# Optimization experiments

Measured on AMD Instinct MI355X. Metric: run time of the kernel, lower is better.

Reference implementation:

```python
import jax, jax.numpy as jnp
import numpy as np

SHIFTS = (1, 2, 4, 8)
NL = 8  # num_layer: 8 fixed contrast kernels


def _base_kernels():
    d1 = np.array([[[-1, 0, 0], [0, 1, 0], [0, 0, 0]],
                   [[0, -1, 0], [0, 1, 0], [0, 0, 0]],
                   [[0, 0, -1], [0, 1, 0], [0, 0, 0]],
                   [[0, 0, 0], [0, 1, -1], [0, 0, 0]]], dtype=np.float32).reshape(4, 1, 3, 3)
    d2 = d1[:, :, ::-1, ::-1].copy()
    k = np.concatenate([d1, d2], axis=0)      # [8,1,3,3] fixed contrast kernels
    k0 = k.mean(0, keepdims=True)             # [1,1,3,3] mean kernel (kernel0)
    return jnp.asarray(k), jnp.asarray(k0)


def _depthwise(x, w, dilation):
    # x: [B,C,H,W], w: [C,1,3,3]; torch conv2d(padding='same', groups=C, dilation=d)
    return jax.lax.conv_general_dilated(
        x, w, window_strides=(1, 1), padding='SAME',
        rhs_dilation=(dilation, dilation),
        dimension_numbers=('NCHW', 'OIHW', 'NCHW'),
        feature_group_count=x.shape[1])


def _l2norm(x, eps=1e-12):
    # F.normalize(dim=-1): x / max(||x||_2, eps)
    n = jnp.sqrt(jnp.sum(x * x, axis=-1, keepdims=True))
    return x / jnp.maximum(n, eps)


def setup_inputs() -> dict:
    key = jax.random.key(0)
    ks = jax.random.split(key, 8)
    B, C, H, W = 8, 64, 96, 96
    nh = len(SHIFTS)
    hid = C // nh
    return {
        'cen': jax.random.normal(ks[0], (B, C, H, W), jnp.float32),
        'sum_weights': jax.random.normal(ks[1], (nh, C, 1, 1, 1, 2), jnp.float32),
        'q_w': jax.random.normal(ks[2], (nh, hid, C), jnp.float32) / np.sqrt(C),
        'k_w': jax.random.normal(ks[3], (nh, NL * hid, NL * C), jnp.float32) / np.sqrt(NL * C),
        'v_w': jax.random.normal(ks[4], (nh, NL * hid, NL * C), jnp.float32) / np.sqrt(NL * C),
        'out_w': jax.random.normal(ks[5], (C, C), jnp.float32) / np.sqrt(C),
        'bn_gamma': jnp.ones((C,), jnp.float32),
        'bn_beta': jnp.zeros((C,), jnp.float32),
    }


def reference(cen, sum_weights, q_w, k_w, v_w, out_w, bn_gamma, bn_beta):
    b, c, h, w = cen.shape
    nh = len(SHIFTS)
    K, K0 = _base_kernels()  # [8,1,3,3], [1,1,3,3]

    keys, qrys, vals = [], [], []
    for i, s in enumerate(SHIFTS):
        sw = jax.nn.softmax(sum_weights[i], axis=-1)  # [C,1,1,1,2]
        # mixed kernels: kernel_j*sw0 + kernel0*sw1 per channel -> [8,C,1,3,3]
        mixed = K[:, None] * sw[None, ..., 0] + K0[:, None] * sw[None, ..., 1]
        # 8 depthwise dilated convs, vmapped over the 8 kernels -> [8,B,C,H,W]
        surr = jax.vmap(lambda kw: _depthwise(cen, kw, s))(mixed)
        # torch.cat along channels in kernel-major order (j, c)
        surr = jnp.transpose(surr, (1, 0, 2, 3, 4)).reshape(b, NL * c, h, w)
        keys.append(jnp.einsum('oc,bchw->bohw', k_w[i], surr))
        vals.append(jnp.einsum('oc,bchw->bohw', v_w[i], surr))
        qrys.append(jnp.einsum('oc,bchw->bohw', q_w[i], cen))

    # torch: stack(dim=2).view(b, nh, -1, h*w)  (raw row-major reinterpret)
    keys = jnp.stack(keys, axis=2).reshape(b, nh, -1, h * w)
    qrys = jnp.stack(qrys, axis=2).reshape(b, nh, -1, h * w)
    vals = jnp.stack(vals, axis=2).reshape(b, nh, -1, h * w)

    k_n = _l2norm(keys)  # L2 norm over spatial axis
    q_n = _l2norm(qrys)
    # scores: [b, heads, hid, 8*hid]
    scores = jnp.einsum('bhqs,bhks->bhqk', q_n, k_n) / jnp.sqrt(jnp.float32(h * w))
    # InstanceNorm2d(num_heads), affine=False, eps=1e-5: per (b, head) over (q, k)
    mu = scores.mean(axis=(-2, -1), keepdims=True)
    var = scores.var(axis=(-2, -1), keepdims=True)
    attn = jax.nn.softmax((scores - mu) * jax.lax.rsqrt(var + 1e-5), axis=-1)
    out = jnp.einsum('bhqk,bhks->bhqs', attn, vals).reshape(b, c, h, w)

    # out_conv: 1x1 conv (no bias) + BatchNorm2d (train-mode batch stats) + ReLU
    y = jnp.einsum('oc,bchw->bohw', out_w, out)
    m = y.mean(axis=(0, 2, 3), keepdims=True)
    v2 = y.var(axis=(0, 2, 3), keepdims=True)
    y = (y - m) * jax.lax.rsqrt(v2 + 1e-5)
    y = y * bn_gamma[None, :, None, None] + bn_beta[None, :, None, None]
    return jax.nn.relu(y)
```

## Files before the change

### kernel.cpp

```cpp
#include <hip/hip_runtime.h>
#include <hip/hip_bf16.h>


#define WS_CEN    0UL
#define WS_SPART  12845056UL
#define WS_W      25690112UL
#define WS_Q      28049408UL
#define WS_KV     46923776UL
#define WS_KKP    197918720UL
#define WS_QQP    198213632UL
#define WS_ATTN   198250496UL
#define WS_OUT    198512640UL
#define WS_BN     217387008UL

typedef __attribute__((ext_vector_type(8))) short short8;
typedef __attribute__((ext_vector_type(4))) float f32x4;

__device__ __forceinline__ float bflo(unsigned int u){ return __uint_as_float(u<<16); }
__device__ __forceinline__ float bfhi(unsigned int u){ return __uint_as_float(u & 0xffff0000u); }
__device__ __forceinline__ unsigned short f2bf(float f){
  unsigned int u = __float_as_uint(f);
  return (unsigned short)((u + 0x7fffu + ((u>>16)&1u)) >> 16);
}
__device__ __forceinline__ unsigned short fbits(float f){
  __hip_bfloat16 h = __float2bfloat16(f);
  return __builtin_bit_cast(unsigned short, h);
}

__global__ __launch_bounds__(256) void pad_kernel(const float* __restrict__ cen, unsigned short* __restrict__ cenbf){
  int idx = blockIdx.x*256 + threadIdx.x;
  int px = idx % 112; int t = idx / 112; int py = t % 112; int bc = t / 112;
  int y = py - 8, x = px - 8;
  float v = 0.f;
  if (y >= 0 && y < 96 && x >= 0 && x < 96) v = cen[(size_t)bc*9216 + y*96 + x];
  cenbf[idx] = fbits(v);
}

__global__ __launch_bounds__(256) void prep_kernel(const float* __restrict__ sumw,
    const float* __restrict__ kw, const float* __restrict__ vw, unsigned short* __restrict__ Wb){
  int idx = blockIdx.x*256 + threadIdx.x;
  int o = idx & 255; int r = idx >> 8; int c = r & 63; r >>= 6; int t = r % 9; int i = r / 9;
  float l0 = sumw[(i*64 + c)*2 + 0], l1 = sumw[(i*64 + c)*2 + 1];
  float m = fmaxf(l0, l1);
  float e0 = expf(l0 - m), e1 = expf(l1 - m);
  float inv = 1.f/(e0 + e1);
  float sw0 = e0*inv, sw1 = e1*inv;
  const float* wsrc = (o < 128) ? (kw + ((size_t)i*128 + o)*512 + c)
                                : (vw + ((size_t)i*128 + (o-128))*512 + c);
  float A = 0.f;
  #pragma unroll
  for (int j = 0; j < 8; ++j) A += wsrc[j*64];
  float val;
  if (t == 4) {
    val = A;
  } else {
    const int tmap[9] = {0,1,2,7,0,3,6,5,4};
    int j = tmap[t];
    val = -(wsrc[j*64]*sw0 + A*sw1*0.125f);
  }
  int k = t*64 + c;
  Wb[(((size_t)i*18 + (k>>5))*256 + o)*32 + (k&31)] = f2bf(val);
}

__global__ __launch_bounds__(256) void qproj_kernel(const float* __restrict__ cen,
    const float* __restrict__ qw, unsigned short* __restrict__ qbf){
  __shared__ float WT[64][64];
  int tid = threadIdx.x;
  int st = blockIdx.x, b = blockIdx.y;
  #pragma unroll
  for (int e = 0; e < 16; ++e) {
    int f = e*256 + tid; int c = f >> 6, row = f & 63;
    int i = row & 3, o = row >> 2;
    WT[c][row] = qw[(size_t)i*1024 + o*64 + c];
  }
  __syncthreads();
  int s = st*256 + tid;
  float acc[64];
  #pragma unroll
  for (int r = 0; r < 64; ++r) acc[r] = 0.f;
  const float* cb = cen + (size_t)b*64*9216 + s;
  for (int c = 0; c < 64; ++c) {
    float xv = cb[(size_t)c*9216];
    #pragma unroll
    for (int r4 = 0; r4 < 16; ++r4) {
      float4 w = *(const float4*)&WT[c][r4*4];
      acc[r4*4+0] = fmaf(w.x, xv, acc[r4*4+0]);
      acc[r4*4+1] = fmaf(w.y, xv, acc[r4*4+1]);
      acc[r4*4+2] = fmaf(w.z, xv, acc[r4*4+2]);
      acc[r4*4+3] = fmaf(w.w, xv, acc[r4*4+3]);
    }
  }
  unsigned short* qb = qbf + (size_t)b*64*9216 + s;
  #pragma unroll
  for (int r = 0; r < 64; ++r) qb[(size_t)r*9216] = fbits(acc[r]);
}

__global__ __launch_bounds__(512, 2) void conv_kv_mfma(const unsigned short* __restrict__ cenbf,
    const unsigned short* __restrict__ Wb, unsigned short* __restrict__ KV){
  __shared__ char Xs[2][256*72];
  const int tid = threadIdx.x;
  const int st = blockIdx.x, ib = blockIdx.z;
  const int i = ib >> 3, b = ib & 7;
  const int dil = 1 << i;
  const int s0 = st*256;
  const int wave = tid >> 6, lane = tid & 63;
  const int wm = wave >> 2, wn = wave & 3;
  const int l15 = lane & 15, l4 = lane >> 4;
  const int s_idx = tid & 255;
  const int khalf = tid >> 8;
  const int s = s0 + s_idx;
  const int y = s / 96, x = s - y*96;
  const unsigned short* cb = cenbf + (size_t)b*802816 + (size_t)(y+8)*112 + (x+8);

  f32x4 acc[8][4];
  #pragma unroll
  for (int mf = 0; mf < 8; ++mf)
    #pragma unroll
    for (int nf = 0; nf < 4; ++nf)
      acc[mf][nf] = (f32x4){0.f, 0.f, 0.f, 0.f};

  const unsigned short* Wi = Wb + (size_t)i*18*8192;
  const unsigned short* apb = Wi + (size_t)(wm*128 + l15)*32 + l4*8;

  unsigned short vs[16];
  auto gather = [&](int kn){
    int t = kn >> 1;
    int cbase = (kn & 1)*32 + khalf*16;
    int dy = (t/3 - 1)*dil, dx = (t - (t/3)*3 - 1)*dil;
    const unsigned short* p = cb + (size_t)cbase*12544 + (dy*112 + dx);
    #pragma unroll
    for (int j = 0; j < 16; ++j) vs[j] = p[(size_t)j*12544];
  };

  gather(0);
  int buf = 0;
  for (int kc = 0; kc < 18; ++kc) {
    short8 a[8];
    const unsigned short* ap = apb + (size_t)kc*8192;
    #pragma unroll
    for (int mf = 0; mf < 8; ++mf) a[mf] = *(const short8*)(ap + mf*512);
    asm volatile("" ::: "memory");
    char* wp = Xs[buf] + s_idx*72 + khalf*32;
    #pragma unroll
    for (int w = 0; w < 4; ++w) {
      unsigned int p0 = (unsigned int)vs[4*w+0] | ((unsigned int)vs[4*w+1] << 16);
      unsigned int p1 = (unsigned int)vs[4*w+2] | ((unsigned int)vs[4*w+3] << 16);
      *(uint2*)(wp + w*8) = make_uint2(p0, p1);
    }
    if (kc < 17) gather(kc + 1);
    asm volatile("s_waitcnt lgkmcnt(0)" ::: "memory");
    __builtin_amdgcn_s_barrier();
    asm volatile("" ::: "memory");
    short8 bfr[4];
    #pragma unroll
    for (int nf = 0; nf < 4; ++nf) {
      const char* rp = Xs[buf] + (wn*64 + nf*16 + l15)*72 + l4*16;
      uint2 lo = *(const uint2*)rp;
      uint2 hi = *(const uint2*)(rp + 8);
      uint4 tb = make_uint4(lo.x, lo.y, hi.x, hi.y);
      bfr[nf] = *(short8*)&tb;
    }
    #pragma unroll
    for (int mf = 0; mf < 8; ++mf)
      #pragma unroll
      for (int nf = 0; nf < 4; ++nf)
        acc[mf][nf] = __builtin_amdgcn_mfma_f32_16x16x32_bf16(a[mf], bfr[nf], acc[mf][nf], 0, 0, 0);
    buf ^= 1;
  }

  #pragma unroll
  for (int mf = 0; mf < 8; ++mf) {
    #pragma unroll
    for (int nf = 0; nf < 4; ++nf) {
      int scol = s0 + wn*64 + nf*16 + l15;
      int obase = wm*128 + mf*16 + l4*4;
      #pragma unroll
      for (int r = 0; r < 4; ++r)
        KV[((size_t)ib*256 + obase + r)*9216 + scol] = fbits(acc[mf][nf][r]);
    }
  }
}

__global__ __launch_bounds__(256) void scores_mfma(const unsigned short* __restrict__ KV,
    const unsigned short* __restrict__ qbf, float* __restrict__ spart,
    float* __restrict__ kkpart, float* __restrict__ qqpart){
  __shared__ float red[4][2192];
  const int tid = threadIdx.x;
  const int chunk = blockIdx.x, hh = blockIdx.y, b = blockIdx.z;
  const int wave = tid >> 6, lane = tid & 63;
  const int l15 = lane & 15, l4 = lane >> 4;
  const int sbase = chunk*512 + wave*128;

  const unsigned short* qp = qbf + ((size_t)(b*64 + hh*16 + l15))*9216 + sbase + l4*8;
  const unsigned short* kp = KV + ((size_t)(((l15&3)*8 + b)*256 + hh*32 + (l15>>2)))*9216 + sbase + l4*8;

  f32x4 sacc[8], kkacc[8], qqacc;
  #pragma unroll
  for (int nf = 0; nf < 8; ++nf) { sacc[nf] = (f32x4){0,0,0,0}; kkacc[nf] = (f32x4){0,0,0,0}; }
  qqacc = (f32x4){0,0,0,0};

  #pragma unroll
  for (int sl = 0; sl < 4; ++sl) {
    short8 qf = *(const short8*)(qp + sl*32);
    short8 kf[8];
    #pragma unroll
    for (int nf = 0; nf < 8; ++nf) kf[nf] = *(const short8*)(kp + (size_t)nf*36864 + sl*32);
    qqacc = __builtin_amdgcn_mfma_f32_16x16x32_bf16(qf, qf, qqacc, 0, 0, 0);
    #pragma unroll
    for (int nf = 0; nf < 8; ++nf) {
      sacc[nf]  = __builtin_amdgcn_mfma_f32_16x16x32_bf16(qf, kf[nf], sacc[nf], 0, 0, 0);
      kkacc[nf] = __builtin_amdgcn_mfma_f32_16x16x32_bf16(kf[nf], kf[nf], kkacc[nf], 0, 0, 0);
    }
  }
  float* rw = red[wave];
  #pragma unroll
  for (int nf = 0; nf < 8; ++nf)
    #pragma unroll
    for (int r = 0; r < 4; ++r)
      rw[(l4*4 + r)*128 + nf*16 + l15] = sacc[nf][r];
  if ((l15 >> 2) == l4) {
    int r = l15 & 3;
    #pragma unroll
    for (int nf = 0; nf < 8; ++nf) rw[2048 + nf*16 + l15] = kkacc[nf][r];
    rw[2176 + l15] = qqacc[r];
  }
  __syncthreads();
  int pb = (b*4 + hh)*18 + chunk;
  for (int t = tid; t < 2192; t += 256) {
    float v = red[0][t] + red[1][t] + red[2][t] + red[3][t];
    if (t < 2048)       spart[(size_t)pb*2048 + t] = v;
    else if (t < 2176)  kkpart[(size_t)pb*128 + (t - 2048)] = v;
    else                qqpart[(size_t)pb*16 + (t - 2176)] = v;
  }
}

__global__ __launch_bounds__(256) void softmax_kernel(const float* __restrict__ spart,
    const float* __restrict__ kkpart, const float* __restrict__ qqpart, float* __restrict__ attnT){
  const int pb = blockIdx.x, tid = threadIdx.x;
  const int qr = tid >> 4, g = tid & 15;
  __shared__ float kkl[128];
  __shared__ float qql[16];
  __shared__ float red[8];
  __shared__ float stats[2];
  float sv[8] = {0,0,0,0,0,0,0,0};
  for (int ch = 0; ch < 18; ++ch) {
    const float* p = spart + ((size_t)(pb*18 + ch))*2048 + qr*128 + g*8;
    #pragma unroll
    for (int e = 0; e < 8; ++e) sv[e] += p[e];
  }
  if (tid < 128) { float ssum = 0.f; for (int ch = 0; ch < 18; ++ch) ssum += kkpart[(size_t)(pb*18+ch)*128 + tid]; kkl[tid] = ssum; }
  if (tid < 16)  { float ssum = 0.f; for (int ch = 0; ch < 18; ++ch) ssum += qqpart[(size_t)(pb*18+ch)*16 + tid]; qql[tid] = ssum; }
  __syncthreads();
  float qn = fmaxf(sqrtf(qql[qr]), 1e-12f);
  float lsum = 0.f, lsq = 0.f;
  #pragma unroll
  for (int e = 0; e < 8; ++e) {
    float kn = fmaxf(sqrtf(kkl[g*8+e]), 1e-12f);
    float v = sv[e] / (qn * kn * 96.0f);
    sv[e] = v; lsum += v; lsq += v*v;
  }
  #pragma unroll
  for (int m = 1; m <= 32; m <<= 1) { lsum += __shfl_xor(lsum, m); lsq += __shfl_xor(lsq, m); }
  if ((tid & 63) == 0) { red[tid >> 6] = lsum; red[4 + (tid >> 6)] = lsq; }
  __syncthreads();
  if (tid == 0) {
    float ts = red[0]+red[1]+red[2]+red[3];
    float tq = red[4]+red[5]+red[6]+red[7];
    float mean = ts / 2048.0f;
    float var = tq / 2048.0f - mean*mean;
    stats[0] = mean; stats[1] = rsqrtf(var + 1e-5f);
  }
  __syncthreads();
  float mean = stats[0], inv = stats[1];
  float mx = -1e30f;
  #pragma unroll
  for (int e = 0; e < 8; ++e) { sv[e] = (sv[e] - mean) * inv; mx = fmaxf(mx, sv[e]); }
  #pragma unroll
  for (int m = 1; m <= 8; m <<= 1) mx = fmaxf(mx, __shfl_xor(mx, m));
  float es = 0.f;
  #pragma unroll
  for (int e = 0; e < 8; ++e) { sv[e] = expf(sv[e] - mx); es += sv[e]; }
  #pragma unroll
  for (int m = 1; m <= 8; m <<= 1) es += __shfl_xor(es, m);
  float rinv = 1.0f / es;
  #pragma unroll
  for (int e = 0; e < 8; ++e) attnT[(size_t)pb*2048 + (g*8+e)*16 + qr] = sv[e] * rinv;
}

__global__ __launch_bounds__(256) void pv_kernel(const unsigned short* __restrict__ KV,
    const float* __restrict__ attnT, float* __restrict__ outbuf){
  __shared__ float at[128][16];
  int tid = threadIdx.x;
  int st = blockIdx.x, hh = blockIdx.y, b = blockIdx.z;
  const float* ap = attnT + ((size_t)(b*4 + hh))*2048;
  #pragma unroll
  for (int e = 0; e < 8; ++e) ((float*)at)[e*256 + tid] = ap[e*256 + tid];
  __syncthreads();
  int sbase = st*1024 + tid*4;
  float acc[16][4];
  #pragma unroll
  for (int q = 0; q < 16; ++q)
    #pragma unroll
    for (int p = 0; p < 4; ++p) acc[q][p] = 0.f;
  #pragma unroll 2
  for (int kr = 0; kr < 128; ++kr) {
    int ii = kr & 3, oo = 128 + hh*32 + (kr >> 2);
    const unsigned short* vp = KV + ((size_t)((ii*8 + b)*256 + oo))*9216 + sbase;
    uint2 u = *(const uint2*)vp;
    float v0 = bflo(u.x), v1 = bfhi(u.x), v2 = bflo(u.y), v3 = bfhi(u.y);
    #pragma unroll
    for (int q4 = 0; q4 < 4; ++q4) {
      float4 a = *(const float4*)&at[kr][q4*4];
      float av[4] = {a.x, a.y, a.z, a.w};
      #pragma unroll
      for (int j = 0; j < 4; ++j) {
        acc[q4*4+j][0] = fmaf(av[j], v0, acc[q4*4+j][0]);
        acc[q4*4+j][1] = fmaf(av[j], v1, acc[q4*4+j][1]);
        acc[q4*4+j][2] = fmaf(av[j], v2, acc[q4*4+j][2]);
        acc[q4*4+j][3] = fmaf(av[j], v3, acc[q4*4+j][3]);
      }
    }
  }
  float* ob = outbuf + ((size_t)(b*64 + hh*16))*9216 + sbase;
  #pragma unroll
  for (int q = 0; q < 16; ++q) {
    float4 w = make_float4(acc[q][0], acc[q][1], acc[q][2], acc[q][3]);
    *(float4*)(ob + (size_t)q*9216) = w;
  }
}

__global__ __launch_bounds__(256) void outconv_kernel(const float* __restrict__ outbuf,
    const float* __restrict__ ow, float* __restrict__ dout){
  __shared__ float WT[64][64];
  int tid = threadIdx.x; int st = blockIdx.x; int b = blockIdx.y;
  #pragma unroll
  for (int e = 0; e < 16; ++e) {
    int f = e*256 + tid; int c = f >> 6, o = f & 63;
    WT[c][o] = ow[o*64 + c];
  }
  __syncthreads();
  int s = st*256 + tid;
  float acc[64];
  #pragma unroll
  for (int o = 0; o < 64; ++o) acc[o] = 0.f;
  for (int c = 0; c < 64; ++c) {
    float xv = outbuf[((size_t)(b*64 + c))*9216 + s];
    #pragma unroll
    for (int o4 = 0; o4 < 16; ++o4) {
      float4 w = *(const float4*)&WT[c][o4*4];
      acc[o4*4+0] = fmaf(w.x, xv, acc[o4*4+0]);
      acc[o4*4+1] = fmaf(w.y, xv, acc[o4*4+1]);
      acc[o4*4+2] = fmaf(w.z, xv, acc[o4*4+2]);
      acc[o4*4+3] = fmaf(w.w, xv, acc[o4*4+3]);
    }
  }
  #pragma unroll
  for (int o = 0; o < 64; ++o) dout[((size_t)(b*64 + o))*9216 + s] = acc[o];
}

__global__ __launch_bounds__(256) void bnstats_kernel(const float* __restrict__ yb, float* __restrict__ bnpart){
  int o = blockIdx.x, qt = blockIdx.y, tid = threadIdx.x;
  float s = 0.f, sq = 0.f;
  for (int k = tid; k < 18432; k += 256) {
    int f = qt*18432 + k;
    int b = f / 9216, sp = f - b*9216;
    float v = yb[((size_t)(b*64 + o))*9216 + sp];
    s += v; sq += v*v;
  }
  #pragma unroll
  for (int m = 1; m <= 32; m <<= 1) { s += __shfl_xor(s, m); sq += __shfl_xor(sq, m); }
  __shared__ float r0[4], r1[4];
  if ((tid & 63) == 0) { r0[tid >> 6] = s; r1[tid >> 6] = sq; }
  __syncthreads();
  if (tid == 0) {
    bnpart[qt*128 + o]      = r0[0]+r0[1]+r0[2]+r0[3];
    bnpart[qt*128 + 64 + o] = r1[0]+r1[1]+r1[2]+r1[3];
  }
}

__global__ __launch_bounds__(256) void bnapply_kernel(float* __restrict__ yb,
    const float* __restrict__ bnpart, const float* __restrict__ gamma, const float* __restrict__ beta){
  int gid = blockIdx.x*256 + threadIdx.x;
  int o = (gid / 2304) & 63;
  float ts = 0.f, tq = 0.f;
  #pragma unroll
  for (int qt = 0; qt < 4; ++qt) { ts += bnpart[qt*128 + o]; tq += bnpart[qt*128 + 64 + o]; }
  float mean = ts * (1.f/73728.f);
  float var = tq * (1.f/73728.f) - mean*mean;
  float inv = rsqrtf(var + 1e-5f);
  float g = gamma[o], be = beta[o];
  float4 v = ((const float4*)yb)[gid];
  v.x = fmaxf((v.x - mean)*inv*g + be, 0.f);
  v.y = fmaxf((v.y - mean)*inv*g + be, 0.f);
  v.z = fmaxf((v.z - mean)*inv*g + be, 0.f);
  v.w = fmaxf((v.w - mean)*inv*g + be, 0.f);
  ((float4*)yb)[gid] = v;
}

extern "C" void kernel_launch(void* const* d_in, const int* in_sizes, int n_in,
                              void* d_out, int out_size, void* d_ws, size_t ws_size,
                              hipStream_t stream) {
  const float* cen   = (const float*)d_in[0];
  const float* sumw  = (const float*)d_in[1];
  const float* qw    = (const float*)d_in[2];
  const float* kw    = (const float*)d_in[3];
  const float* vw    = (const float*)d_in[4];
  const float* ow    = (const float*)d_in[5];
  const float* gamma = (const float*)d_in[6];
  const float* beta  = (const float*)d_in[7];

  char* ws = (char*)d_ws;
  unsigned short* cenbf  = (unsigned short*)(ws + WS_CEN);
  float*          spart  = (float*)(ws + WS_SPART);
  unsigned short* Wb     = (unsigned short*)(ws + WS_W);
  unsigned short* qbf    = (unsigned short*)(ws + WS_Q);
  unsigned short* KV     = (unsigned short*)(ws + WS_KV);
  float*          kkp    = (float*)(ws + WS_KKP);
  float*          qqp    = (float*)(ws + WS_QQP);
  float*          attnT  = (float*)(ws + WS_ATTN);
  float*          outbuf = (float*)(ws + WS_OUT);
  float*          bnp    = (float*)(ws + WS_BN);

  pad_kernel    <<<25088, 256, 0, stream>>>(cen, cenbf);
  prep_kernel   <<<2304, 256, 0, stream>>>(sumw, kw, vw, Wb);
  qproj_kernel  <<<dim3(36, 8), 256, 0, stream>>>(cen, qw, qbf);
  conv_kv_mfma  <<<dim3(36, 1, 32), 512, 0, stream>>>(cenbf, Wb, KV);
  scores_mfma   <<<dim3(18, 4, 8), 256, 0, stream>>>(KV, qbf, spart, kkp, qqp);
  softmax_kernel<<<32, 256, 0, stream>>>(spart, kkp, qqp, attnT);
  pv_kernel     <<<dim3(9, 4, 8), 256, 0, stream>>>(KV, attnT, outbuf);
  outconv_kernel<<<dim3(36, 8), 256, 0, stream>>>(outbuf, ow, (float*)d_out);
  bnstats_kernel<<<dim3(64, 4), 256, 0, stream>>>((const float*)d_out, bnp);
  bnapply_kernel<<<4608, 256, 0, stream>>>((float*)d_out, bnp, gamma, beta);
}
```

Before: 441.9 us.

## Fold out_conv weights into attention, fuse PV+outconv+BN stats via MFMA GEMM

Result: faster. 427.7 us (-3.2%).

```diff
diff --git a/kernel.cpp b/kernel.cpp
--- a/kernel.cpp
+++ b/kernel.cpp
@@ -10,8 +10,9 @@
 #define WS_KKP    197918720UL
 #define WS_QQP    198213632UL
 #define WS_ATTN   198250496UL
-#define WS_OUT    198512640UL
-#define WS_BN     217387008UL
+#define WS_AB     198512640UL
+#define WS_BNP    217387008UL
+#define WS_BNF    217681920UL
 
 typedef __attribute__((ext_vector_type(8))) short short8;
 typedef __attribute__((ext_vector_type(4))) float f32x4;
@@ -95,32 +96,32 @@
   for (int r = 0; r < 64; ++r) qb[(size_t)r*9216] = fbits(acc[r]);
 }
 
-__global__ __launch_bounds__(512, 2) void conv_kv_mfma(const unsigned short* __restrict__ cenbf,
+__global__ __launch_bounds__(256, 3) void conv_kv_mfma(const unsigned short* __restrict__ cenbf,
     const unsigned short* __restrict__ Wb, unsigned short* __restrict__ KV){
-  __shared__ char Xs[2][256*72];
+  __shared__ char Xs[2][128*72];
   const int tid = threadIdx.x;
-  const int st = blockIdx.x, ib = blockIdx.z;
+  const int st = blockIdx.x, oc = blockIdx.y, ib = blockIdx.z;
   const int i = ib >> 3, b = ib & 7;
   const int dil = 1 << i;
-  const int s0 = st*256;
+  const int s0 = st*128;
   const int wave = tid >> 6, lane = tid & 63;
-  const int wm = wave >> 2, wn = wave & 3;
+  const int wm = wave >> 1, wn = wave & 1;
   const int l15 = lane & 15, l4 = lane >> 4;
-  const int s_idx = tid & 255;
-  const int khalf = tid >> 8;
+  const int s_idx = tid & 127;
+  const int khalf = tid >> 7;
   const int s = s0 + s_idx;
   const int y = s / 96, x = s - y*96;
   const unsigned short* cb = cenbf + (size_t)b*802816 + (size_t)(y+8)*112 + (x+8);
 
-  f32x4 acc[8][4];
-  #pragma unroll
-  for (int mf = 0; mf < 8; ++mf)
+  f32x4 acc[4][4];
+  #pragma unroll
+  for (int mf = 0; mf < 4; ++mf)
     #pragma unroll
     for (int nf = 0; nf < 4; ++nf)
       acc[mf][nf] = (f32x4){0.f, 0.f, 0.f, 0.f};
 
   const unsigned short* Wi = Wb + (size_t)i*18*8192;
-  const unsigned short* apb = Wi + (size_t)(wm*128 + l15)*32 + l4*8;
+  const unsigned short* apb = Wi + (size_t)(oc*128 + wm*64 + l15)*32 + l4*8;
 
   unsigned short vs[16];
   auto gather = [&](int kn){
@@ -135,10 +136,10 @@
   gather(0);
   int buf = 0;
   for (int kc = 0; kc < 18; ++kc) {
-    short8 a[8];
+    short8 a[4];
     const unsigned short* ap = apb + (size_t)kc*8192;
     #pragma unroll
-    for (int mf = 0; mf < 8; ++mf) a[mf] = *(const short8*)(ap + mf*512);
+    for (int mf = 0; mf < 4; ++mf) a[mf] = *(const short8*)(ap + mf*512);
     asm volatile("" ::: "memory");
     char* wp = Xs[buf] + s_idx*72 + khalf*32;
     #pragma unroll
@@ -161,7 +162,7 @@
       bfr[nf] = *(short8*)&tb;
     }
     #pragma unroll
-    for (int mf = 0; mf < 8; ++mf)
+    for (int mf = 0; mf < 4; ++mf)
       #pragma unroll
       for (int nf = 0; nf < 4; ++nf)
         acc[mf][nf] = __builtin_amdgcn_mfma_f32_16x16x32_bf16(a[mf], bfr[nf], acc[mf][nf], 0, 0, 0);
@@ -169,11 +170,11 @@
   }
 
   #pragma unroll
-  for (int mf = 0; mf < 8; ++mf) {
+  for (int mf = 0; mf < 4; ++mf) {
     #pragma unroll
     for (int nf = 0; nf < 4; ++nf) {
       int scol = s0 + wn*64 + nf*16 + l15;
-      int obase = wm*128 + mf*16 + l4*4;
+      int obase = oc*128 + wm*64 + mf*16 + l4*4;
       #pragma unroll
       for (int r = 0; r < 4; ++r)
         KV[((size_t)ib*256 + obase + r)*9216 + scol] = fbits(acc[mf][nf][r]);
@@ -287,106 +288,124 @@
   for (int e = 0; e < 8; ++e) attnT[(size_t)pb*2048 + (g*8+e)*16 + qr] = sv[e] * rinv;
 }
 
-__global__ __launch_bounds__(256) void pv_kernel(const unsigned short* __restrict__ KV,
-    const float* __restrict__ attnT, float* __restrict__ outbuf){
-  __shared__ float at[128][16];
-  int tid = threadIdx.x;
-  int st = blockIdx.x, hh = blockIdx.y, b = blockIdx.z;
-  const float* ap = attnT + ((size_t)(b*4 + hh))*2048;
-  #pragma unroll
-  for (int e = 0; e < 8; ++e) ((float*)at)[e*256 + tid] = ap[e*256 + tid];
-  __syncthreads();
-  int sbase = st*1024 + tid*4;
-  float acc[16][4];
-  #pragma unroll
-  for (int q = 0; q < 16; ++q)
-    #pragma unroll
-    for (int p = 0; p < 4; ++p) acc[q][p] = 0.f;
-  #pragma unroll 2
-  for (int kr = 0; kr < 128; ++kr) {
-    int ii = kr & 3, oo = 128 + hh*32 + (kr >> 2);
-    const unsigned short* vp = KV + ((size_t)((ii*8 + b)*256 + oo))*9216 + sbase;
-    uint2 u = *(const uint2*)vp;
-    float v0 = bflo(u.x), v1 = bfhi(u.x), v2 = bflo(u.y), v3 = bfhi(u.y);
-    #pragma unroll
-    for (int q4 = 0; q4 < 4; ++q4) {
-      float4 a = *(const float4*)&at[kr][q4*4];
-      float av[4] = {a.x, a.y, a.z, a.w};
+__global__ __launch_bounds__(256) void attnfold_kernel(const float* __restrict__ attnT,
+    const float* __restrict__ ow, unsigned short* __restrict__ Ab){
+  int idx = blockIdx.x*256 + threadIdx.x;
+  int kr = idx & 127, hh = (idx >> 7) & 3, o2 = (idx >> 9) & 63, b = idx >> 15;
+  const float* ap = attnT + ((size_t)(b*4 + hh))*2048 + kr*16;
+  const float* wp = ow + o2*64 + hh*16;
+  float acc = 0.f;
+  #pragma unroll
+  for (int qr = 0; qr < 16; ++qr) acc += wp[qr] * ap[qr];
+  int rc = (kr & 3)*4 + hh, ch = kr >> 2;
+  Ab[(((size_t)b*16 + rc)*64 + o2)*32 + ch] = fbits(acc);
+}
+
+__global__ __launch_bounds__(256, 3) void ygemm_kernel(const unsigned short* __restrict__ KV,
+    const unsigned short* __restrict__ Ab, float* __restrict__ dout, float* __restrict__ bnpart){
+  __shared__ char Xs[2][128*72];
+  __shared__ float bns[4][32], bnq[4][32];
+  const int tid = threadIdx.x;
+  const int st = blockIdx.x, b = blockIdx.y;
+  const int wave = tid >> 6, lane = tid & 63;
+  const int wm = wave >> 1, wn = wave & 1;
+  const int l15 = lane & 15, l4 = lane >> 4;
+  const int s_idx = tid & 127, khalf = tid >> 7;
+  const int s0 = st*128;
+
+  f32x4 acc[2][4];
+  #pragma unroll
+  for (int mf = 0; mf < 2; ++mf)
+    #pragma unroll
+    for (int nf = 0; nf < 4; ++nf)
+      acc[mf][nf] = (f32x4){0.f, 0.f, 0.f, 0.f};
+
+  const unsigned short* Abb = Ab + ((size_t)b*16*64)*32 + (size_t)(wm*32 + l15)*32 + l4*8;
+
+  unsigned short vs[16];
+  auto vgather = [&](int kn){
+    int vr = (((kn >> 2)*8 + b)*256 + 128 + (kn & 3)*32) + khalf*16;
+    const unsigned short* p = KV + (size_t)vr*9216 + s0 + s_idx;
+    #pragma unroll
+    for (int j = 0; j < 16; ++j) vs[j] = p[(size_t)j*9216];
+  };
+
+  vgather(0);
+  int buf = 0;
+  for (int kc = 0; kc < 16; ++kc) {
+    short8 a[2];
+    #pragma unroll
+    for (int mf = 0; mf < 2; ++mf) a[mf] = *(const short8*)(Abb + (size_t)kc*2048 + mf*512);
+    asm volatile("" ::: "memory");
+    char* wp = Xs[buf] + s_idx*72 + khalf*32;
+    #pragma unroll
+    for (int w = 0; w < 4; ++w) {
+      unsigned int p0 = (unsigned int)vs[4*w+0] | ((unsigned int)vs[4*w+1] << 16);
+      unsigned int p1 = (unsigned int)vs[4*w+2] | ((unsigned int)vs[4*w+3] << 16);
+      *(uint2*)(wp + w*8) = make_uint2(p0, p1);
+    }
+    if (kc < 15) vgather(kc + 1);
+    asm volatile("s_waitcnt lgkmcnt(0)" ::: "memory");
+    __builtin_amdgcn_s_barrier();
+    asm volatile("" ::: "memory");
+    short8 bfr[4];
+    #pragma unroll
+    for (int nf = 0; nf < 4; ++nf) {
+      const char* rp = Xs[buf] + (wn*64 + nf*16 + l15)*72 + l4*16;
+      uint2 lo = *(const uint2*)rp;
+      uint2 hi = *(const uint2*)(rp + 8);
+      uint4 tb = make_uint4(lo.x, lo.y, hi.x, hi.y);
+      bfr[nf] = *(short8*)&tb;
+    }
+    #pragma unroll
+    for (int mf = 0; mf < 2; ++mf)
       #pragma unroll
-      for (int j = 0; j < 4; ++j) {
-        acc[q4*4+j][0] = fmaf(av[j], v0, acc[q4*4+j][0]);
-        acc[q4*4+j][1] = fmaf(av[j], v1, acc[q4*4+j][1]);
-        acc[q4*4+j][2] = fmaf(av[j], v2, acc[q4*4+j][2]);
-        acc[q4*4+j][3] = fmaf(av[j], v3, acc[q4*4+j][3]);
+      for (int nf = 0; nf < 4; ++nf)
+        acc[mf][nf] = __builtin_amdgcn_mfma_f32_16x16x32_bf16(a[mf], bfr[nf], acc[mf][nf], 0, 0, 0);
+    buf ^= 1;
+  }
+
+  #pragma unroll
+  for (int mf = 0; mf < 2; ++mf) {
+    #pragma unroll
+    for (int rr = 0; rr < 4; ++rr) {
+      int o2 = wm*32 + mf*16 + l4*4 + rr;
+      float vsum = 0.f, vsq = 0.f;
+      #pragma unroll
+      for (int nf = 0; nf < 4; ++nf) {
+        float v = acc[mf][nf][rr];
+        vsum += v; vsq += v*v;
+        dout[((size_t)(b*64 + o2))*9216 + s0 + wn*64 + nf*16 + l15] = v;
       }
-    }
-  }
-  float* ob = outbuf + ((size_t)(b*64 + hh*16))*9216 + sbase;
-  #pragma unroll
-  for (int q = 0; q < 16; ++q) {
-    float4 w = make_float4(acc[q][0], acc[q][1], acc[q][2], acc[q][3]);
-    *(float4*)(ob + (size_t)q*9216) = w;
-  }
-}
-
-__global__ __launch_bounds__(256) void outconv_kernel(const float* __restrict__ outbuf,
-    const float* __restrict__ ow, float* __restrict__ dout){
-  __shared__ float WT[64][64];
-  int tid = threadIdx.x; int st = blockIdx.x; int b = blockIdx.y;
-  #pragma unroll
-  for (int e = 0; e < 16; ++e) {
-    int f = e*256 + tid; int c = f >> 6, o = f & 63;
-    WT[c][o] = ow[o*64 + c];
-  }
-  __syncthreads();
-  int s = st*256 + tid;
-  float acc[64];
-  #pragma unroll
-  for (int o = 0; o < 64; ++o) acc[o] = 0.f;
-  for (int c = 0; c < 64; ++c) {
-    float xv = outbuf[((size_t)(b*64 + c))*9216 + s];
-    #pragma unroll
-    for (int o4 = 0; o4 < 16; ++o4) {
-      float4 w = *(const float4*)&WT[c][o4*4];
-      acc[o4*4+0] = fmaf(w.x, xv, acc[o4*4+0]);
-      acc[o4*4+1] = fmaf(w.y, xv, acc[o4*4+1]);
-      acc[o4*4+2] = fmaf(w.z, xv, acc[o4*4+2]);
-      acc[o4*4+3] = fmaf(w.w, xv, acc[o4*4+3]);
-    }
-  }
-  #pragma unroll
-  for (int o = 0; o < 64; ++o) dout[((size_t)(b*64 + o))*9216 + s] = acc[o];
-}
-
-__global__ __launch_bounds__(256) void bnstats_kernel(const float* __restrict__ yb, float* __restrict__ bnpart){
-  int o = blockIdx.x, qt = blockIdx.y, tid = threadIdx.x;
-  float s = 0.f, sq = 0.f;
-  for (int k = tid; k < 18432; k += 256) {
-    int f = qt*18432 + k;
-    int b = f / 9216, sp = f - b*9216;
-    float v = yb[((size_t)(b*64 + o))*9216 + sp];
-    s += v; sq += v*v;
-  }
-  #pragma unroll
-  for (int m = 1; m <= 32; m <<= 1) { s += __shfl_xor(s, m); sq += __shfl_xor(sq, m); }
-  __shared__ float r0[4], r1[4];
-  if ((tid & 63) == 0) { r0[tid >> 6] = s; r1[tid >> 6] = sq; }
-  __syncthreads();
-  if (tid == 0) {
-    bnpart[qt*128 + o]      = r0[0]+r0[1]+r0[2]+r0[3];
-    bnpart[qt*128 + 64 + o] = r1[0]+r1[1]+r1[2]+r1[3];
-  }
+      #pragma unroll
+      for (int m = 1; m <= 8; m <<= 1) { vsum += __shfl_xor(vsum, m); vsq += __shfl_xor(vsq, m); }
+      if (l15 == 0) { bns[wave][mf*16 + l4*4 + rr] = vsum; bnq[wave][mf*16 + l4*4 + rr] = vsq; }
+    }
+  }
+  __syncthreads();
+  if (tid < 64) {
+    int wmq = tid >> 5, local = tid & 31;
+    float s_ = bns[wmq*2][local] + bns[wmq*2+1][local];
+    float q_ = bnq[wmq*2][local] + bnq[wmq*2+1][local];
+    int bid = b*72 + st;
+    bnpart[(size_t)bid*128 + tid] = s_;
+    bnpart[(size_t)bid*128 + 64 + tid] = q_;
+  }
+}
+
+__global__ __launch_bounds__(128) void bncombine_kernel(const float* __restrict__ bnpart, float* __restrict__ bnfin){
+  int t = threadIdx.x;
+  float a = 0.f;
+  for (int blk = 0; blk < 576; ++blk) a += bnpart[(size_t)blk*128 + t];
+  bnfin[t] = a;
 }
 
 __global__ __launch_bounds__(256) void bnapply_kernel(float* __restrict__ yb,
-    const float* __restrict__ bnpart, const float* __restrict__ gamma, const float* __restrict__ beta){
+    const float* __restrict__ bnfin, const float* __restrict__ gamma, const float* __restrict__ beta){
   int gid = blockIdx.x*256 + threadIdx.x;
   int o = (gid / 2304) & 63;
-  float ts = 0.f, tq = 0.f;
-  #pragma unroll
-  for (int qt = 0; qt < 4; ++qt) { ts += bnpart[qt*128 + o]; tq += bnpart[qt*128 + 64 + o]; }
-  float mean = ts * (1.f/73728.f);
-  float var = tq * (1.f/73728.f) - mean*mean;
+  float mean = bnfin[o] * (1.f/73728.f);
+  float var = bnfin[64 + o] * (1.f/73728.f) - mean*mean;
   float inv = rsqrtf(var + 1e-5f);
   float g = gamma[o], be = beta[o];
   float4 v = ((const float4*)yb)[gid];
@@ -418,17 +437,18 @@
   float*          kkp    = (float*)(ws + WS_KKP);
   float*          qqp    = (float*)(ws + WS_QQP);
   float*          attnT  = (float*)(ws + WS_ATTN);
-  float*          outbuf = (float*)(ws + WS_OUT);
-  float*          bnp    = (float*)(ws + WS_BN);
-
-  pad_kernel    <<<25088, 256, 0, stream>>>(cen, cenbf);
-  prep_kernel   <<<2304, 256, 0, stream>>>(sumw, kw, vw, Wb);
-  qproj_kernel  <<<dim3(36, 8), 256, 0, stream>>>(cen, qw, qbf);
-  conv_kv_mfma  <<<dim3(36, 1, 32), 512, 0, stream>>>(cenbf, Wb, KV);
-  scores_mfma   <<<dim3(18, 4, 8), 256, 0, stream>>>(KV, qbf, spart, kkp, qqp);
-  softmax_kernel<<<32, 256, 0, stream>>>(spart, kkp, qqp, attnT);
-  pv_kernel     <<<dim3(9, 4, 8), 256, 0, stream>>>(KV, attnT, outbuf);
-  outconv_kernel<<<dim3(36, 8), 256, 0, stream>>>(outbuf, ow, (float*)d_out);
-  bnstats_kernel<<<dim3(64, 4), 256, 0, stream>>>((const float*)d_out, bnp);
-  bnapply_kernel<<<4608, 256, 0, stream>>>((float*)d_out, bnp, gamma, beta);
-}
+  unsigned short* Ab     = (unsigned short*)(ws + WS_AB);
+  float*          bnp    = (float*)(ws + WS_BNP);
+  float*          bnf    = (float*)(ws + WS_BNF);
+
+  pad_kernel     <<<25088, 256, 0, stream>>>(cen, cenbf);
+  prep_kernel    <<<2304, 256, 0, stream>>>(sumw, kw, vw, Wb);
+  qproj_kernel   <<<dim3(36, 8), 256, 0, stream>>>(cen, qw, qbf);
+  conv_kv_mfma   <<<dim3(72, 2, 32), 256, 0, stream>>>(cenbf, Wb, KV);
+  scores_mfma    <<<dim3(18, 4, 8), 256, 0, stream>>>(KV, qbf, spart, kkp, qqp);
+  softmax_kernel <<<32, 256, 0, stream>>>(spart, kkp, qqp, attnT);
+  attnfold_kernel<<<1024, 256, 0, stream>>>(attnT, ow, Ab);
+  ygemm_kernel   <<<dim3(72, 8), 256, 0, stream>>>(KV, Ab, (float*)d_out, bnp);
+  bncombine_kernel<<<1, 128, 0, stream>>>(bnp, bnf);
+  bnapply_kernel <<<4608, 256, 0, stream>>>((float*)d_out, bnf, gamma, beta);
+}
```
